# Performance work log

Measured on AMD Instinct MI355X. Metric: run time of the kernel, lower is better.

The kernel has to match this reference:

```python
import jax, jax.numpy as jnp
import numpy as np

ALPHA = 0.2       # LeakyReLU negative slope
OUT_FEATURES = 256
NEG_INF = -9e15   # matches -9000000000000000.0 in the torch code

N = 8192
IN_FEATURES = 512


def setup_inputs() -> dict:
    key = jax.random.key(0)
    k1, k2, k3, k4 = jax.random.split(key, 4)
    h = jax.random.normal(k1, (N, IN_FEATURES), dtype=jnp.float32)
    adj = jax.random.randint(k2, (N, N), 0, 2, dtype=jnp.int32)
    # xavier-uniform-like init scales (exact init values don't matter for correctness)
    W = jax.random.normal(k3, (IN_FEATURES, OUT_FEATURES), dtype=jnp.float32) * 0.05
    a = jax.random.normal(k4, (2 * OUT_FEATURES, 1), dtype=jnp.float32) * 0.05
    return {"h": h, "adj": adj, "W": W, "a": a, "split_name": 0}


def reference(h, adj, W, a, split_name):
    # h: [N, Fin], W: [Fin, Fout], a: [2*Fout, 1], adj: [N, N]
    Wh = h @ W                                   # [N, Fout]
    Wh1 = Wh @ a[:OUT_FEATURES, :]               # [N, 1]
    Wh2 = Wh @ a[OUT_FEATURES:, :]               # [N, 1]
    e = jax.nn.leaky_relu(Wh1 + Wh2.T, negative_slope=ALPHA)  # [N, N]
    mask = adj > 0
    scores = jnp.where(mask, e, jnp.float32(NEG_INF))
    attention = jax.nn.softmax(scores, axis=1)
    # dropout is identity in eval mode (training=False)
    attention = jnp.where(mask, attention, jnp.float32(0.0))
    h_prime = attention @ Wh                     # [N, Fout]
    return jax.nn.elu(h_prime)                   # concat=True -> elu
```

## Files before the change

### kernel.cpp

```cpp
#include <hip/hip_runtime.h>

#define NN 8192
#define FIN 512
#define FOUT 256
#define JS 8
#define STRIP 1024
#define NSTEP 32

typedef _Float16 f16;
typedef __attribute__((ext_vector_type(8))) _Float16 f16x8;
typedef __attribute__((ext_vector_type(4))) _Float16 f16x4;
typedef __attribute__((ext_vector_type(4))) float f32x4;
typedef __attribute__((ext_vector_type(16))) float f32x16;
typedef __attribute__((ext_vector_type(4))) int i32x4;
typedef unsigned long long u64;

__device__ __forceinline__ float lrelu(float x) { return fmaxf(x, 0.2f * x); }

__global__ void k_convert(const int* __restrict__ adj, u64* __restrict__ maskG) {
  int gw = blockIdx.x * 4 + (threadIdx.x >> 6);
  int l = threadIdx.x & 63;
  const int* src = adj + (size_t)gw * NN + 4 * l;
  u64* dst = maskG + (size_t)gw * 128;
#pragma unroll 1
  for (int p = 0; p < 32; ++p) {
    i32x4 v = __builtin_nontemporal_load((const i32x4*)(src + p * 256));
    u64 b0 = __ballot(v[0] > 0);
    u64 b1 = __ballot(v[1] > 0);
    u64 b2 = __ballot(v[2] > 0);
    u64 b3 = __ballot(v[3] > 0);
    if (l < 4) {
      u64 bb = (l == 0) ? b0 : (l == 1) ? b1 : (l == 2) ? b2 : b3;
      dst[p * 4 + l] = bb;
    }
  }
}

__global__ void k_prep_w(const float* __restrict__ W, f16* __restrict__ wth,
                         f16* __restrict__ wtl) {
  int id = blockIdx.x * 256 + threadIdx.x;
  int c = id >> 9, k = id & 511;
  float v = W[k * FOUT + c];
  f16 a = (f16)v;
  wth[c * FIN + k] = a;
  wtl[c * FIN + k] = (f16)(v - (float)a);
}

__launch_bounds__(256, 2)
__global__ void k_gemm1(const float* __restrict__ h, const f16* __restrict__ wth,
                        const f16* __restrict__ wtl, const float* __restrict__ avec,
                        f16* __restrict__ whT16, float* __restrict__ wh1,
                        float* __restrict__ wh2) {
  int i0 = blockIdx.x * 32;
  int tid = threadIdx.x;
  int w = tid >> 6, l = tid & 63, m = l & 15, g = l >> 4;
  f32x4 acc[2][4] = {};
#pragma unroll 1
  for (int k0 = 0; k0 < FIN; k0 += 32) {
    f16x8 ah[2], al[2], bh[4], bl[4];
#pragma unroll
    for (int rf = 0; rf < 2; ++rf) {
      int ro = (i0 + 16 * rf + m) * FIN + k0 + 8 * g;
      f32x4 va = *(const f32x4*)(h + ro);
      f32x4 vb = *(const f32x4*)(h + ro + 4);
#pragma unroll
      for (int e = 0; e < 4; ++e) {
        f16 x = (f16)va[e];
        ah[rf][e] = x;
        al[rf][e] = (f16)(va[e] - (float)x);
        f16 y = (f16)vb[e];
        ah[rf][4 + e] = y;
        al[rf][4 + e] = (f16)(vb[e] - (float)y);
      }
    }
#pragma unroll
    for (int cf = 0; cf < 4; ++cf) {
      int co = (64 * w + 16 * cf + m) * FIN + k0 + 8 * g;
      bh[cf] = *(const f16x8*)(wth + co);
      bl[cf] = *(const f16x8*)(wtl + co);
    }
#pragma unroll
    for (int rf = 0; rf < 2; ++rf)
#pragma unroll
      for (int cf = 0; cf < 4; ++cf) {
        acc[rf][cf] = __builtin_amdgcn_mfma_f32_16x16x32_f16(ah[rf], bh[cf], acc[rf][cf], 0, 0, 0);
        acc[rf][cf] = __builtin_amdgcn_mfma_f32_16x16x32_f16(ah[rf], bl[cf], acc[rf][cf], 0, 0, 0);
        acc[rf][cf] = __builtin_amdgcn_mfma_f32_16x16x32_f16(al[rf], bh[cf], acc[rf][cf], 0, 0, 0);
      }
  }
  __shared__ float tile[32][FOUT + 1];
#pragma unroll
  for (int rf = 0; rf < 2; ++rf)
#pragma unroll
    for (int cf = 0; cf < 4; ++cf)
#pragma unroll
      for (int r = 0; r < 4; ++r)
        tile[16 * rf + 4 * g + r][64 * w + 16 * cf + m] = acc[rf][cf][r];
  __syncthreads();
  {
    int c = tid;
    f16x8 vv[4];
#pragma unroll
    for (int r = 0; r < 32; ++r) vv[r >> 3][r & 7] = (f16)tile[r][c];
    size_t base = ((size_t)(i0 >> 4) * 256 + c) * 16;
    *(f16x8*)(whT16 + base) = vv[0];
    *(f16x8*)(whT16 + base + 8) = vv[1];
    *(f16x8*)(whT16 + base + 4096) = vv[2];
    *(f16x8*)(whT16 + base + 4096 + 8) = vv[3];
  }
  {
    int r = tid >> 3, ls = tid & 7;
    float s1 = 0.f, s2 = 0.f;
    for (int c = ls; c < FOUT; c += 8) {
      float v = tile[r][c];
      s1 = fmaf(v, avec[c], s1);
      s2 = fmaf(v, avec[FOUT + c], s2);
    }
#pragma unroll
    for (int off = 1; off < 8; off <<= 1) {
      s1 += __shfl_xor(s1, off);
      s2 += __shfl_xor(s2, off);
    }
    if (ls == 0) {
      wh1[i0 + r] = s1;
      wh2[i0 + r] = s2;
    }
  }
}

__global__ void k_max2(const float* __restrict__ wh2, float* __restrict__ m2) {
  int t = threadIdx.x;
  float mx = -1e30f;
  for (int i = t; i < NN; i += 256) mx = fmaxf(mx, wh2[i]);
#pragma unroll
  for (int off = 1; off < 64; off <<= 1) mx = fmaxf(mx, __shfl_xor(mx, off));
  __shared__ float sm[4];
  if ((t & 63) == 0) sm[t >> 6] = mx;
  __syncthreads();
  if (t == 0) m2[0] = fmaxf(fmaxf(sm[0], sm[1]), fmaxf(sm[2], sm[3]));
}

__global__ void k_prep2(const float* __restrict__ wh1, const float* __restrict__ wh2,
                        const float* __restrict__ m2g, float* __restrict__ e1p,
                        float* __restrict__ e1n, float* __restrict__ thr,
                        float* __restrict__ e2p, float* __restrict__ e2n) {
  int i = blockIdx.x * 256 + threadIdx.x;
  const float L = 1.4426950408889634f;
  float M2 = m2g[0];
  float w1 = wh1[i], w2 = wh2[i];
  float m = lrelu(w1 + M2);
  e1p[i] = exp2f((w1 - m) * L);
  e1n[i] = exp2f((0.2f * w1 - m) * L);
  thr[i] = exp2f(-w1 * L);
  e2p[i] = exp2f(w2 * L);
  e2n[i] = exp2f(0.2f * w2 * L);
}

__launch_bounds__(256, 2)
__global__ void k_attn(const u64* __restrict__ maskG, const f16* __restrict__ whT16,
                       const float* __restrict__ e1pA, const float* __restrict__ e1nA,
                       const float* __restrict__ thrA, const float* __restrict__ e2pA,
                       const float* __restrict__ e2nA, f16* __restrict__ accP,
                       float* __restrict__ zP) {
  int bx = blockIdx.x;
  int js = bx & (JS - 1), rb = bx >> 3;
  int i0b = rb * 128;
  int jbase = js * STRIP;
  int tid = threadIdx.x, w = tid >> 6, l = tid & 63;
  int lr = l & 31, hi = l >> 5;
  int row = i0b + w * 32 + lr;

  __shared__ u64 mrow[4][32][18];
#pragma unroll
  for (int p = 0; p < 4; ++p) {
    int r = 8 * p + (l >> 3);
    const i32x4* src =
        (const i32x4*)(maskG + (size_t)(i0b + 32 * w + r) * 128 + js * 16) + (l & 7);
    *(i32x4*)(&mrow[w][r][(l & 7) * 2]) = *src;
  }

  float E1p = e1pA[row], E1n = e1nA[row], T = thrA[row];
  f32x16 acc[8] = {};
  float za = 0.f;

  const f16* bPB = whT16 + ((size_t)(jbase >> 4)) * 256 * 16 + (size_t)lr * 16 + hi * 8;
  const float* e2pb = e2pA + jbase + 8 * hi;
  const float* e2nb = e2nA + jbase + 8 * hi;

  f16x8 bfA[8], bfB[8];
#pragma unroll
  for (int c = 0; c < 8; ++c) bfA[c] = *(const f16x8*)(bPB + c * 512);

#pragma unroll 1
  for (int ch = 0; ch < 4; ++ch) {
    u64 wreg[4];
#pragma unroll
    for (int q = 0; q < 4; ++q) wreg[q] = mrow[w][lr][ch * 4 + q];
#pragma unroll 1
    for (int ts = 0; ts < 8; ++ts) {
      int t = ch * 8 + ts;
      int jc = t * 32;
      {
        const f16* bt = bPB + (size_t)(2 * t + 1) * 4096;
#pragma unroll
        for (int c = 0; c < 8; ++c) bfB[c] = *(const f16x8*)(bt + c * 512);
      }
      int sb = ts * 8 + 2 * hi;
      unsigned b4[4];
#pragma unroll
      for (int e = 0; e < 4; ++e) b4[e] = (unsigned)(wreg[e] >> sb);
      f16x8 pa0, pa1;
#pragma unroll
      for (int q = 0; q < 2; ++q) {
        int fo = jc + 4 * q;
        f32x4 ep0 = *(const f32x4*)(e2pb + fo);
        f32x4 en0 = *(const f32x4*)(e2nb + fo);
        f32x4 ep1 = *(const f32x4*)(e2pb + fo + 16);
        f32x4 en1 = *(const f32x4*)(e2nb + fo + 16);
#pragma unroll
        for (int e = 0; e < 4; ++e) {
          int f = 4 * q + e;
          bool s0 = ep0[e] >= T;
          float pv0 = (s0 ? E1p : E1n) * (s0 ? ep0[e] : en0[e]);
          pv0 = ((b4[e] >> q) & 1u) ? pv0 : 0.f;
          za += pv0;
          pa0[f] = (f16)pv0;
          bool s1 = ep1[e] >= T;
          float pv1 = (s1 ? E1p : E1n) * (s1 ? ep1[e] : en1[e]);
          pv1 = ((b4[e] >> (4 + q)) & 1u) ? pv1 : 0.f;
          za += pv1;
          pa1[f] = (f16)pv1;
        }
      }
#pragma unroll
      for (int c = 0; c < 8; ++c)
        acc[c] = __builtin_amdgcn_mfma_f32_32x32x16_f16(pa0, bfA[c], acc[c], 0, 0, 0);
      {
        int tn = (t + 1 < NSTEP) ? t + 1 : t;
        const f16* bt = bPB + (size_t)(2 * tn) * 4096;
#pragma unroll
        for (int c = 0; c < 8; ++c) bfA[c] = *(const f16x8*)(bt + c * 512);
      }
#pragma unroll
      for (int c = 0; c < 8; ++c)
        acc[c] = __builtin_amdgcn_mfma_f32_32x32x16_f16(pa1, bfB[c], acc[c], 0, 0, 0);
    }
  }

  za += __shfl_xor(za, 32);
  if (hi == 0) zP[(size_t)js * NN + row] = za;

  f16* ap = accP + (size_t)js * NN * FOUT;
#pragma unroll
  for (int c = 0; c < 8; ++c)
#pragma unroll
    for (int r = 0; r < 16; ++r) {
      int grow = i0b + 32 * w + (r & 3) + 8 * (r >> 2) + 4 * hi;
      int gcol = c * 32 + lr;
      __builtin_nontemporal_store((f16)acc[c][r], ap + (size_t)grow * FOUT + gcol);
    }
}

__global__ void k_combine(const f16* __restrict__ accP, const float* __restrict__ zP,
                          float* __restrict__ out) {
  int id = blockIdx.x * 256 + threadIdx.x;
  size_t idx = (size_t)id * 4;
  int row = (int)(idx >> 8);
  f32x4 s = {};
#pragma unroll
  for (int p = 0; p < JS; ++p) {
    f16x4 v = *(const f16x4*)(accP + (size_t)p * NN * FOUT + idx);
#pragma unroll
    for (int i = 0; i < 4; ++i) s[i] += (float)v[i];
  }
  float z = 0.f;
#pragma unroll
  for (int p = 0; p < JS; ++p) z += zP[(size_t)p * NN + row];
  float inv = (z > 0.f) ? 1.f / z : 0.f;
  f32x4 o;
#pragma unroll
  for (int i = 0; i < 4; ++i) {
    float x = s[i] * inv;
    o[i] = (x > 0.f) ? x : expm1f(x);
  }
  *(f32x4*)(out + idx) = o;
}

extern "C" void kernel_launch(void* const* d_in, const int* in_sizes, int n_in,
                              void* d_out, int out_size, void* d_ws, size_t ws_size,
                              hipStream_t stream) {
  const float* h = (const float*)d_in[0];
  const int* adj = (const int*)d_in[1];
  const float* W = (const float*)d_in[2];
  const float* a = (const float*)d_in[3];
  (void)in_sizes; (void)n_in; (void)out_size; (void)ws_size;

  char* ws = (char*)d_ws;
  size_t off = 0;
  auto alloc = [&](size_t bytes) {
    void* p = ws + off;
    off = (off + bytes + 255) & ~(size_t)255;
    return p;
  };
  f16* accP = (f16*)alloc((size_t)JS * NN * FOUT * 2);
  u64* maskG = (u64*)alloc((size_t)NN * 128 * 8);
  f16* whT16 = (f16*)alloc((size_t)FOUT * NN * 2);
  f16* wth = (f16*)alloc((size_t)FOUT * FIN * 2);
  f16* wtl = (f16*)alloc((size_t)FOUT * FIN * 2);
  float* wh1 = (float*)alloc((size_t)NN * 4);
  float* wh2 = (float*)alloc((size_t)NN * 4);
  float* m2 = (float*)alloc(256);
  float* e1p = (float*)alloc((size_t)NN * 4);
  float* e1n = (float*)alloc((size_t)NN * 4);
  float* thr = (float*)alloc((size_t)NN * 4);
  float* e2p = (float*)alloc((size_t)NN * 4);
  float* e2n = (float*)alloc((size_t)NN * 4);
  float* zP = (float*)alloc((size_t)JS * NN * 4);

  k_convert<<<NN / 4, 256, 0, stream>>>(adj, maskG);
  k_prep_w<<<FIN * FOUT / 256, 256, 0, stream>>>(W, wth, wtl);
  k_gemm1<<<NN / 32, 256, 0, stream>>>(h, wth, wtl, a, whT16, wh1, wh2);
  k_max2<<<1, 256, 0, stream>>>(wh2, m2);
  k_prep2<<<NN / 256, 256, 0, stream>>>(wh1, wh2, m2, e1p, e1n, thr, e2p, e2n);
  k_attn<<<(NN / 128) * JS, 256, 0, stream>>>(maskG, whT16, e1p, e1n, thr, e2p, e2n,
                                              accP, zP);
  k_combine<<<NN * FOUT / 1024, 256, 0, stream>>>(accP, zP, (float*)d_out);
}
```

Measured before the change: 156.0 us.

## Retile attention warps to 64x128 tiles and software-pipeline adjacency loads in mask conversion

Each warp in the attention kernel now covers 64 rows by 128 output columns, where it previously covered 32 rows by all 256 columns. This halves the per-warp B-fragment loads of Wh and reuses each fragment across two MFMA row groups. The cost is that the probability computation is now done twice, once per column-half warp pair, and the mask shared-memory buffer doubles in size. The mask conversion kernel also prefetches adjacency rows two iterations ahead to hide global load latency.

New measurement: 158.5 us. No clear change (+1.6%).

```diff
diff --git a/kernel.cpp b/kernel.cpp
--- a/kernel.cpp
+++ b/kernel.cpp
@@ -22,17 +22,23 @@
   int l = threadIdx.x & 63;
   const int* src = adj + (size_t)gw * NN + 4 * l;
   u64* dst = maskG + (size_t)gw * 128;
+  i32x4 v0 = __builtin_nontemporal_load((const i32x4*)src);
+  i32x4 v1 = __builtin_nontemporal_load((const i32x4*)(src + 256));
 #pragma unroll 1
   for (int p = 0; p < 32; ++p) {
-    i32x4 v = __builtin_nontemporal_load((const i32x4*)(src + p * 256));
-    u64 b0 = __ballot(v[0] > 0);
-    u64 b1 = __ballot(v[1] > 0);
-    u64 b2 = __ballot(v[2] > 0);
-    u64 b3 = __ballot(v[3] > 0);
+    i32x4 nx = (p + 2 < 32)
+                   ? __builtin_nontemporal_load((const i32x4*)(src + (p + 2) * 256))
+                   : v1;
+    u64 b0 = __ballot(v0[0] > 0);
+    u64 b1 = __ballot(v0[1] > 0);
+    u64 b2 = __ballot(v0[2] > 0);
+    u64 b3 = __ballot(v0[3] > 0);
     if (l < 4) {
       u64 bb = (l == 0) ? b0 : (l == 1) ? b1 : (l == 2) ? b2 : b3;
       dst[p * 4 + l] = bb;
     }
+    v0 = v1;
+    v1 = nx;
   }
 }
 
@@ -168,34 +174,40 @@
   int jbase = js * STRIP;
   int tid = threadIdx.x, w = tid >> 6, l = tid & 63;
   int lr = l & 31, hi = l >> 5;
-  int row = i0b + w * 32 + lr;
-
-  __shared__ u64 mrow[4][32][18];
-#pragma unroll
-  for (int p = 0; p < 4; ++p) {
+  int ch2 = w & 1, rh = w >> 1;
+  int r0 = i0b + rh * 64 + lr;
+
+  __shared__ u64 mrow[4][64][18];
+#pragma unroll
+  for (int p = 0; p < 8; ++p) {
     int r = 8 * p + (l >> 3);
     const i32x4* src =
-        (const i32x4*)(maskG + (size_t)(i0b + 32 * w + r) * 128 + js * 16) + (l & 7);
+        (const i32x4*)(maskG + (size_t)(i0b + rh * 64 + r) * 128 + js * 16) + (l & 7);
     *(i32x4*)(&mrow[w][r][(l & 7) * 2]) = *src;
   }
 
-  float E1p = e1pA[row], E1n = e1nA[row], T = thrA[row];
-  f32x16 acc[8] = {};
-  float za = 0.f;
-
-  const f16* bPB = whT16 + ((size_t)(jbase >> 4)) * 256 * 16 + (size_t)lr * 16 + hi * 8;
+  float E1pa = e1pA[r0], E1na = e1nA[r0], Ta = thrA[r0];
+  float E1pb = e1pA[r0 + 32], E1nb = e1nA[r0 + 32], Tb = thrA[r0 + 32];
+  f32x16 acc[2][4] = {};
+  float za = 0.f, zb = 0.f;
+
+  const f16* bPB = whT16 + ((size_t)(jbase >> 4)) * 256 * 16 +
+                   (size_t)(ch2 * 128 + lr) * 16 + hi * 8;
   const float* e2pb = e2pA + jbase + 8 * hi;
   const float* e2nb = e2nA + jbase + 8 * hi;
 
-  f16x8 bfA[8], bfB[8];
-#pragma unroll
-  for (int c = 0; c < 8; ++c) bfA[c] = *(const f16x8*)(bPB + c * 512);
+  f16x8 bfA[4], bfB[4];
+#pragma unroll
+  for (int c = 0; c < 4; ++c) bfA[c] = *(const f16x8*)(bPB + c * 512);
 
 #pragma unroll 1
   for (int ch = 0; ch < 4; ++ch) {
-    u64 wreg[4];
-#pragma unroll
-    for (int q = 0; q < 4; ++q) wreg[q] = mrow[w][lr][ch * 4 + q];
+    u64 wr0[4], wr1[4];
+#pragma unroll
+    for (int q = 0; q < 4; ++q) {
+      wr0[q] = mrow[w][lr][ch * 4 + q];
+      wr1[q] = mrow[w][32 + lr][ch * 4 + q];
+    }
 #pragma unroll 1
     for (int ts = 0; ts < 8; ++ts) {
       int t = ch * 8 + ts;
@@ -203,13 +215,16 @@
       {
         const f16* bt = bPB + (size_t)(2 * t + 1) * 4096;
 #pragma unroll
-        for (int c = 0; c < 8; ++c) bfB[c] = *(const f16x8*)(bt + c * 512);
+        for (int c = 0; c < 4; ++c) bfB[c] = *(const f16x8*)(bt + c * 512);
       }
       int sb = ts * 8 + 2 * hi;
-      unsigned b4[4];
-#pragma unroll
-      for (int e = 0; e < 4; ++e) b4[e] = (unsigned)(wreg[e] >> sb);
-      f16x8 pa0, pa1;
+      unsigned a4[4], b4[4];
+#pragma unroll
+      for (int e = 0; e < 4; ++e) {
+        a4[e] = (unsigned)(wr0[e] >> sb);
+        b4[e] = (unsigned)(wr1[e] >> sb);
+      }
+      f16x8 pa00, pa01, pa10, pa11;
 #pragma unroll
       for (int q = 0; q < 2; ++q) {
         int fo = jc + 4 * q;
@@ -220,45 +235,65 @@
 #pragma unroll
         for (int e = 0; e < 4; ++e) {
           int f = 4 * q + e;
-          bool s0 = ep0[e] >= T;
-          float pv0 = (s0 ? E1p : E1n) * (s0 ? ep0[e] : en0[e]);
-          pv0 = ((b4[e] >> q) & 1u) ? pv0 : 0.f;
-          za += pv0;
-          pa0[f] = (f16)pv0;
-          bool s1 = ep1[e] >= T;
-          float pv1 = (s1 ? E1p : E1n) * (s1 ? ep1[e] : en1[e]);
-          pv1 = ((b4[e] >> (4 + q)) & 1u) ? pv1 : 0.f;
-          za += pv1;
-          pa1[f] = (f16)pv1;
+          bool s0 = ep0[e] >= Ta;
+          float v0 = (s0 ? E1pa : E1na) * (s0 ? ep0[e] : en0[e]);
+          v0 = ((a4[e] >> q) & 1u) ? v0 : 0.f;
+          za += v0;
+          pa00[f] = (f16)v0;
+          bool s1 = ep1[e] >= Ta;
+          float v1 = (s1 ? E1pa : E1na) * (s1 ? ep1[e] : en1[e]);
+          v1 = ((a4[e] >> (4 + q)) & 1u) ? v1 : 0.f;
+          za += v1;
+          pa01[f] = (f16)v1;
+          bool s2 = ep0[e] >= Tb;
+          float v2 = (s2 ? E1pb : E1nb) * (s2 ? ep0[e] : en0[e]);
+          v2 = ((b4[e] >> q) & 1u) ? v2 : 0.f;
+          zb += v2;
+          pa10[f] = (f16)v2;
+          bool s3 = ep1[e] >= Tb;
+          float v3 = (s3 ? E1pb : E1nb) * (s3 ? ep1[e] : en1[e]);
+          v3 = ((b4[e] >> (4 + q)) & 1u) ? v3 : 0.f;
+          zb += v3;
+          pa11[f] = (f16)v3;
         }
       }
 #pragma unroll
-      for (int c = 0; c < 8; ++c)
-        acc[c] = __builtin_amdgcn_mfma_f32_32x32x16_f16(pa0, bfA[c], acc[c], 0, 0, 0);
+      for (int c = 0; c < 4; ++c) {
+        acc[0][c] = __builtin_amdgcn_mfma_f32_32x32x16_f16(pa00, bfA[c], acc[0][c], 0, 0, 0);
+        acc[1][c] = __builtin_amdgcn_mfma_f32_32x32x16_f16(pa10, bfA[c], acc[1][c], 0, 0, 0);
+      }
       {
         int tn = (t + 1 < NSTEP) ? t + 1 : t;
         const f16* bt = bPB + (size_t)(2 * tn) * 4096;
 #pragma unroll
-        for (int c = 0; c < 8; ++c) bfA[c] = *(const f16x8*)(bt + c * 512);
-      }
-#pragma unroll
-      for (int c = 0; c < 8; ++c)
-        acc[c] = __builtin_amdgcn_mfma_f32_32x32x16_f16(pa1, bfB[c], acc[c], 0, 0, 0);
+        for (int c = 0; c < 4; ++c) bfA[c] = *(const f16x8*)(bt + c * 512);
+      }
+#pragma unroll
+      for (int c = 0; c < 4; ++c) {
+        acc[0][c] = __builtin_amdgcn_mfma_f32_32x32x16_f16(pa01, bfB[c], acc[0][c], 0, 0, 0);
+        acc[1][c] = __builtin_amdgcn_mfma_f32_32x32x16_f16(pa11, bfB[c], acc[1][c], 0, 0, 0);
+      }
     }
   }
 
   za += __shfl_xor(za, 32);
-  if (hi == 0) zP[(size_t)js * NN + row] = za;
+  zb += __shfl_xor(zb, 32);
+  if (hi == 0 && ch2 == 0) {
+    zP[(size_t)js * NN + r0] = za;
+    zP[(size_t)js * NN + r0 + 32] = zb;
+  }
 
   f16* ap = accP + (size_t)js * NN * FOUT;
 #pragma unroll
-  for (int c = 0; c < 8; ++c)
-#pragma unroll
-    for (int r = 0; r < 16; ++r) {
-      int grow = i0b + 32 * w + (r & 3) + 8 * (r >> 2) + 4 * hi;
-      int gcol = c * 32 + lr;
-      __builtin_nontemporal_store((f16)acc[c][r], ap + (size_t)grow * FOUT + gcol);
-    }
+  for (int rg = 0; rg < 2; ++rg)
+#pragma unroll
+    for (int c = 0; c < 4; ++c)
+#pragma unroll
+      for (int r = 0; r < 16; ++r) {
+        int grow = i0b + rh * 64 + rg * 32 + (r & 3) + 8 * (r >> 2) + 4 * hi;
+        int gcol = ch2 * 128 + c * 32 + lr;
+        __builtin_nontemporal_store((f16)acc[rg][c][r], ap + (size_t)grow * FOUT + gcol);
+      }
 }
 
 __global__ void k_combine(const f16* __restrict__ accP, const float* __restrict__ zP,
```

## Stage Wh tiles through double-buffered swizzled LDS, prefetch adj loads, fuse max/prep

Applied to the files above, without the earlier changes.

The attention kernel now loads each Wh tile once per block into a double-buffered, XOR-swizzled LDS buffer and reads the MFMA B fragments from LDS. Previously each of the four waves fetched its B fragments straight from global memory. The adjacency-to-bitmask conversion keeps four loads in flight through a small register ring. The single-block max kernel is merged into the prep kernel, with every block recomputing the global max. In exchange the attention kernel adds 32KB of LDS and a barrier per step, and the prep work now does redundant max reductions.

Result: no change. 155.8 us (-0.1%).

```diff
diff --git a/kernel.cpp b/kernel.cpp
--- a/kernel.cpp
+++ b/kernel.cpp
@@ -22,13 +22,19 @@
   int l = threadIdx.x & 63;
   const int* src = adj + (size_t)gw * NN + 4 * l;
   u64* dst = maskG + (size_t)gw * 128;
+  i32x4 v[4];
+#pragma unroll
+  for (int p = 0; p < 4; ++p)
+    v[p] = __builtin_nontemporal_load((const i32x4*)(src + p * 256));
 #pragma unroll 1
   for (int p = 0; p < 32; ++p) {
-    i32x4 v = __builtin_nontemporal_load((const i32x4*)(src + p * 256));
-    u64 b0 = __ballot(v[0] > 0);
-    u64 b1 = __ballot(v[1] > 0);
-    u64 b2 = __ballot(v[2] > 0);
-    u64 b3 = __ballot(v[3] > 0);
+    i32x4 cur = v[p & 3];
+    u64 b0 = __ballot(cur[0] > 0);
+    u64 b1 = __ballot(cur[1] > 0);
+    u64 b2 = __ballot(cur[2] > 0);
+    u64 b3 = __ballot(cur[3] > 0);
+    if (p + 4 < 32)
+      v[p & 3] = __builtin_nontemporal_load((const i32x4*)(src + (p + 4) * 256));
     if (l < 4) {
       u64 bb = (l == 0) ? b0 : (l == 1) ? b1 : (l == 2) ? b2 : b3;
       dst[p * 4 + l] = bb;
@@ -128,7 +134,10 @@
   }
 }
 
-__global__ void k_max2(const float* __restrict__ wh2, float* __restrict__ m2) {
+__global__ void k_maxprep(const float* __restrict__ wh1, const float* __restrict__ wh2,
+                          float* __restrict__ e1p, float* __restrict__ e1n,
+                          float* __restrict__ thr, float* __restrict__ e2p,
+                          float* __restrict__ e2n) {
   int t = threadIdx.x;
   float mx = -1e30f;
   for (int i = t; i < NN; i += 256) mx = fmaxf(mx, wh2[i]);
@@ -137,16 +146,9 @@
   __shared__ float sm[4];
   if ((t & 63) == 0) sm[t >> 6] = mx;
   __syncthreads();
-  if (t == 0) m2[0] = fmaxf(fmaxf(sm[0], sm[1]), fmaxf(sm[2], sm[3]));
-}
-
-__global__ void k_prep2(const float* __restrict__ wh1, const float* __restrict__ wh2,
-                        const float* __restrict__ m2g, float* __restrict__ e1p,
-                        float* __restrict__ e1n, float* __restrict__ thr,
-                        float* __restrict__ e2p, float* __restrict__ e2n) {
-  int i = blockIdx.x * 256 + threadIdx.x;
+  float M2 = fmaxf(fmaxf(sm[0], sm[1]), fmaxf(sm[2], sm[3]));
   const float L = 1.4426950408889634f;
-  float M2 = m2g[0];
+  int i = blockIdx.x * 256 + t;
   float w1 = wh1[i], w2 = wh2[i];
   float m = lrelu(w1 + M2);
   e1p[i] = exp2f((w1 - m) * L);
@@ -171,6 +173,8 @@
   int row = i0b + w * 32 + lr;
 
   __shared__ u64 mrow[4][32][18];
+  __shared__ __align__(16) char ldsB[2][16384];
+
 #pragma unroll
   for (int p = 0; p < 4; ++p) {
     int r = 8 * p + (l >> 3);
@@ -183,32 +187,48 @@
   f32x16 acc[8] = {};
   float za = 0.f;
 
-  const f16* bPB = whT16 + ((size_t)(jbase >> 4)) * 256 * 16 + (size_t)lr * 16 + hi * 8;
+  const size_t jb16 = (size_t)(jbase >> 4) * 4096;
   const float* e2pb = e2pA + jbase + 8 * hi;
   const float* e2nb = e2nA + jbase + 8 * hi;
 
-  f16x8 bfA[8], bfB[8];
-#pragma unroll
-  for (int c = 0; c < 8; ++c) bfA[c] = *(const f16x8*)(bPB + c * 512);
+  int ldst[4];
+  size_t gsrc[4];
+#pragma unroll
+  for (int r = 0; r < 4; ++r) {
+    int g = r * 256 + tid;
+    gsrc[r] = (size_t)(g >> 9) * 4096 + 8 * (g & 511);
+    ldst[r] = (g >> 9) * 8192 + ((16 * (g & 511)) ^ (((g >> 3) & 7) << 4));
+  }
+  int rdbase = (lr * 32 + hi * 16) ^ (((lr >> 2) & 7) << 4);
+
+  i32x4 stg[4];
+#pragma unroll
+  for (int r = 0; r < 4; ++r)
+    stg[r] = __builtin_nontemporal_load((const i32x4*)(whT16 + jb16 + gsrc[r]));
+#pragma unroll
+  for (int r = 0; r < 4; ++r) *(i32x4*)(&ldsB[0][ldst[r]]) = stg[r];
+  __syncthreads();
 
 #pragma unroll 1
   for (int ch = 0; ch < 4; ++ch) {
-    u64 wreg[4];
-#pragma unroll
-    for (int q = 0; q < 4; ++q) wreg[q] = mrow[w][lr][ch * 4 + q];
+    u64 wr0[4];
+#pragma unroll
+    for (int q = 0; q < 4; ++q) wr0[q] = mrow[w][lr][ch * 4 + q];
 #pragma unroll 1
     for (int ts = 0; ts < 8; ++ts) {
       int t = ch * 8 + ts;
+      int cur = t & 1;
       int jc = t * 32;
-      {
-        const f16* bt = bPB + (size_t)(2 * t + 1) * 4096;
-#pragma unroll
-        for (int c = 0; c < 8; ++c) bfB[c] = *(const f16x8*)(bt + c * 512);
+      if (t + 1 < NSTEP) {
+        const f16* src = whT16 + jb16 + (size_t)(2 * (t + 1)) * 4096;
+#pragma unroll
+        for (int r = 0; r < 4; ++r)
+          stg[r] = __builtin_nontemporal_load((const i32x4*)(src + gsrc[r]));
       }
       int sb = ts * 8 + 2 * hi;
       unsigned b4[4];
 #pragma unroll
-      for (int e = 0; e < 4; ++e) b4[e] = (unsigned)(wreg[e] >> sb);
+      for (int e = 0; e < 4; ++e) b4[e] = (unsigned)(wr0[e] >> sb);
       f16x8 pa0, pa1;
 #pragma unroll
       for (int q = 0; q < 2; ++q) {
@@ -221,29 +241,32 @@
         for (int e = 0; e < 4; ++e) {
           int f = 4 * q + e;
           bool s0 = ep0[e] >= T;
-          float pv0 = (s0 ? E1p : E1n) * (s0 ? ep0[e] : en0[e]);
-          pv0 = ((b4[e] >> q) & 1u) ? pv0 : 0.f;
-          za += pv0;
-          pa0[f] = (f16)pv0;
+          float v0 = (s0 ? E1p : E1n) * (s0 ? ep0[e] : en0[e]);
+          v0 = ((b4[e] >> q) & 1u) ? v0 : 0.f;
+          za += v0;
+          pa0[f] = (f16)v0;
           bool s1 = ep1[e] >= T;
-          float pv1 = (s1 ? E1p : E1n) * (s1 ? ep1[e] : en1[e]);
-          pv1 = ((b4[e] >> (4 + q)) & 1u) ? pv1 : 0.f;
-          za += pv1;
-          pa1[f] = (f16)pv1;
+          float v1 = (s1 ? E1p : E1n) * (s1 ? ep1[e] : en1[e]);
+          v1 = ((b4[e] >> (4 + q)) & 1u) ? v1 : 0.f;
+          za += v1;
+          pa1[f] = (f16)v1;
         }
       }
 #pragma unroll
-      for (int c = 0; c < 8; ++c)
-        acc[c] = __builtin_amdgcn_mfma_f32_32x32x16_f16(pa0, bfA[c], acc[c], 0, 0, 0);
-      {
-        int tn = (t + 1 < NSTEP) ? t + 1 : t;
-        const f16* bt = bPB + (size_t)(2 * tn) * 4096;
-#pragma unroll
-        for (int c = 0; c < 8; ++c) bfA[c] = *(const f16x8*)(bt + c * 512);
-      }
-#pragma unroll
-      for (int c = 0; c < 8; ++c)
-        acc[c] = __builtin_amdgcn_mfma_f32_32x32x16_f16(pa1, bfB[c], acc[c], 0, 0, 0);
+      for (int cf = 0; cf < 8; ++cf) {
+        f16x8 bf0 = *(const f16x8*)(&ldsB[cur][cf * 1024 + rdbase]);
+        acc[cf] = __builtin_amdgcn_mfma_f32_32x32x16_f16(pa0, bf0, acc[cf], 0, 0, 0);
+      }
+#pragma unroll
+      for (int cf = 0; cf < 8; ++cf) {
+        f16x8 bf1 = *(const f16x8*)(&ldsB[cur][8192 + cf * 1024 + rdbase]);
+        acc[cf] = __builtin_amdgcn_mfma_f32_32x32x16_f16(pa1, bf1, acc[cf], 0, 0, 0);
+      }
+      if (t + 1 < NSTEP) {
+#pragma unroll
+        for (int r = 0; r < 4; ++r) *(i32x4*)(&ldsB[cur ^ 1][ldst[r]]) = stg[r];
+        __syncthreads();
+      }
     }
   }
 
@@ -309,7 +332,6 @@
   f16* wtl = (f16*)alloc((size_t)FOUT * FIN * 2);
   float* wh1 = (float*)alloc((size_t)NN * 4);
   float* wh2 = (float*)alloc((size_t)NN * 4);
-  float* m2 = (float*)alloc(256);
   float* e1p = (float*)alloc((size_t)NN * 4);
   float* e1n = (float*)alloc((size_t)NN * 4);
   float* thr = (float*)alloc((size_t)NN * 4);
@@ -320,8 +342,7 @@
   k_convert<<<NN / 4, 256, 0, stream>>>(adj, maskG);
   k_prep_w<<<FIN * FOUT / 256, 256, 0, stream>>>(W, wth, wtl);
   k_gemm1<<<NN / 32, 256, 0, stream>>>(h, wth, wtl, a, whT16, wh1, wh2);
-  k_max2<<<1, 256, 0, stream>>>(wh2, m2);
-  k_prep2<<<NN / 256, 256, 0, stream>>>(wh1, wh2, m2, e1p, e1n, thr, e2p, e2n);
+  k_maxprep<<<NN / 256, 256, 0, stream>>>(wh1, wh2, e1p, e1n, thr, e2p, e2n);
   k_attn<<<(NN / 128) * JS, 256, 0, stream>>>(maskG, whT16, e1p, e1n, thr, e2p, e2n,
                                               accP, zP);
   k_combine<<<NN * FOUT / 1024, 256, 0, stream>>>(accP, zP, (float*)d_out);
```
